# Kernel optimization log

Hardware: AMD Instinct MI355X
Metric: run time of the kernel (lower is better)

Reference implementation:

```python
import jax, jax.numpy as jnp
import numpy as np

N_NODES = 8192
GNN_DIM = 512
N_FEAT = 64
N_ITER = 4


def setup_inputs() -> dict:
    key = jax.random.key(0)
    ks = jax.random.split(key, 8)
    scale = 1.0 / np.sqrt(GNN_DIM)
    return {
        "labels": jax.random.normal(ks[0], (N_NODES, GNN_DIM), dtype=jnp.float32),
        "adj": jax.random.uniform(ks[1], (N_NODES, N_NODES), dtype=jnp.float32),
        "features": jax.random.normal(ks[2], (N_FEAT,), dtype=jnp.float32),
        "W_self": jax.random.normal(ks[3], (GNN_DIM, GNN_DIM), dtype=jnp.float32) * scale,
        "b_self": jax.random.normal(ks[4], (GNN_DIM,), dtype=jnp.float32) * scale,
        "W_neigh": jax.random.normal(ks[5], (GNN_DIM, GNN_DIM), dtype=jnp.float32) * scale,
        "W_fc": jax.random.normal(ks[6], (1, GNN_DIM + N_FEAT), dtype=jnp.float32) * scale,
        "b_fc": jax.random.normal(ks[7], (1,), dtype=jnp.float32) * scale,
    }


def reference(labels, adj, features, W_self, b_self, W_neigh, W_fc, b_fc):
    x = labels  # [N, D]
    for _ in range(N_ITER):
        acc = adj @ x                                   # [N, D] neighbor aggregation
        x = jax.nn.relu(x @ W_self.T + b_self + acc @ W_neigh.T)
    pooled = jnp.mean(x, axis=0)                        # [D]
    z = jnp.concatenate([pooled, features]) @ W_fc.T + b_fc  # [1]
    return jax.nn.sigmoid(z)
```

## Files before the change

kernel.cpp:

```cpp
#include <hip/hip_runtime.h>

typedef __bf16 bf16;
typedef bf16 bf16x8 __attribute__((ext_vector_type(8)));
typedef bf16 bf16x4 __attribute__((ext_vector_type(4)));
typedef float f32x4 __attribute__((ext_vector_type(4)));

constexpr int NN = 8192;
constexpr int DD = 512;
constexpr size_t PSZB = (size_t)NN * DD * 2;
constexpr size_t PSZE = (size_t)NN * DD;
constexpr int NS = 4;

static __device__ inline bf16x8 cvt8(const float* __restrict__ p) {
  f32x4 a = *(const f32x4*)p;
  f32x4 b = *(const f32x4*)(p + 4);
  bf16x8 r;
  r[0] = (bf16)a[0]; r[1] = (bf16)a[1]; r[2] = (bf16)a[2]; r[3] = (bf16)a[3];
  r[4] = (bf16)b[0]; r[5] = (bf16)b[1]; r[6] = (bf16)b[2]; r[7] = (bf16)b[3];
  return r;
}

#define GLDS(g, l) __builtin_amdgcn_global_load_lds( \
    (const __attribute__((address_space(1))) unsigned int*)(const void*)(g), \
    (__attribute__((address_space(3))) unsigned int*)(void*)(l), 16, 0, 0)


__global__ __launch_bounds__(256) void convert_w_kernel(
    const float* __restrict__ a, const float* __restrict__ b,
    bf16* __restrict__ ao, bf16* __restrict__ bo) {
  int i8 = ((int)blockIdx.x * 256 + (int)threadIdx.x) * 8;
  if (i8 < DD * DD) {
    *(bf16x8*)&ao[i8] = cvt8(a + i8);
  } else {
    int j = i8 - DD * DD;
    *(bf16x8*)&bo[j] = cvt8(b + j);
  }
}

__global__ __launch_bounds__(256) void convert_adj_kernel(
    const float* __restrict__ a, bf16* __restrict__ o) {
  size_t i8 = ((size_t)blockIdx.x * 256 + threadIdx.x) * 8;
  *(bf16x8*)&o[i8] = cvt8(a + i8);
}

__global__ __launch_bounds__(256) void convert_x_kernel(
    const float* __restrict__ src, bf16* __restrict__ xb, bf16* __restrict__ xbT) {
  __shared__ __align__(16) float tile[64][68];
  const int tid = (int)threadIdx.x;
  const int r0 = (int)blockIdx.x * 64;
  const int c0 = (int)blockIdx.y * 64;
#pragma unroll
  for (int p = 0; p < 4; ++p) {
    int row = p * 16 + (tid >> 4);
    int col = (tid & 15) * 4;
    *(f32x4*)&tile[row][col] = *(const f32x4*)&src[(size_t)(r0 + row) * DD + c0 + col];
  }
  __syncthreads();
#pragma unroll
  for (int p = 0; p < 4; ++p) {
    int row = p * 16 + (tid >> 4);
    int col = (tid & 15) * 4;
    f32x4 v = *(const f32x4*)&tile[row][col];
    bf16x4 o;
    o[0] = (bf16)v[0]; o[1] = (bf16)v[1]; o[2] = (bf16)v[2]; o[3] = (bf16)v[3];
    *(bf16x4*)&xb[(size_t)(r0 + row) * DD + c0 + col] = o;
  }
  {
    int c = tid >> 2;
    int rp = (tid & 3) * 16;
    bf16x8 o0, o1;
#pragma unroll
    for (int j = 0; j < 8; ++j) o0[j] = (bf16)tile[rp + j][c];
#pragma unroll
    for (int j = 0; j < 8; ++j) o1[j] = (bf16)tile[rp + 8 + j][c];
    *(bf16x8*)&xbT[(size_t)(c0 + c) * NN + r0 + rp] = o0;
    *(bf16x8*)&xbT[(size_t)(c0 + c) * NN + r0 + rp + 8] = o1;
  }
}


__device__ __forceinline__ void stage_half(const bf16* __restrict__ g, int grow0, int k0,
                                           bf16* smbase, int wave, int lane) {
#pragma unroll
  for (int i = 0; i < 2; ++i) {
    int c = wave * 2 + i;
    int row = grow0 + c * 8 + (lane >> 3);
    int col = k0 + (((lane & 7) ^ ((lane >> 3) & 7)) << 3);
    GLDS(g + (size_t)row * NN + col, smbase + c * 512);
  }
}

__global__ __launch_bounds__(512, 2)
void gemm1_kernel(const bf16* __restrict__ adjb, const bf16* __restrict__ xbT,
                  bf16* __restrict__ pbase) {
  __shared__ __align__(16) bf16 sm[65536];
  const int bid  = (int)blockIdx.x;
  const int xcd  = bid & 7, ii = bid >> 3;
  const int cb   = ii & 1;
  const int jj_  = xcd + 8 * (ii >> 1);
  const int p    = jj_ >> 2;
  const int s    = jj_ & 3;
  const int prow0 = p * 256;
  const int bcol0 = cb * 256;
  const int kb    = s * 2048;
  bf16* __restrict__ P = pbase + (size_t)s * PSZE;

  const int tid  = (int)threadIdx.x;
  const int lane = tid & 63;
  const int wave = tid >> 6;
  const int wr   = wave >> 2;
  const int wc   = wave & 3;
  const int fr   = lane & 15, fq = lane >> 4;

  f32x4 acc[8][4] = {};

#define A_OFF(par) ((par) * 32768)
#define B_OFF(par) ((par) * 32768 + 16384)
#define STAGE_A(tile, half, par) \
  stage_half(adjb, prow0 + (half) * 128, kb + ((tile) & 31) * 64, \
             sm + A_OFF(par) + (half) * 8192, wave, lane)
#define STAGE_B(tile, half, par) \
  stage_half(xbT, bcol0 + (half) * 128, kb + ((tile) & 31) * 64, \
             sm + B_OFF(par) + (half) * 8192, wave, lane)
#define BARRIER() __builtin_amdgcn_s_barrier(); __builtin_amdgcn_sched_barrier(0)

  STAGE_B(0, 0, 0); STAGE_B(0, 1, 0); STAGE_A(0, 0, 0); STAGE_A(0, 1, 0);
  STAGE_B(1, 0, 1); STAGE_B(1, 1, 1); STAGE_A(1, 0, 1);

  bf16x8 bv[2][4], af[2][2];

#define LOAD_B(par)                                                        \
  _Pragma("unroll") for (int kk = 0; kk < 2; ++kk)                         \
  _Pragma("unroll") for (int n = 0; n < 4; ++n) {                          \
    int rowl = wc * 64 + n * 16 + fr;                                      \
    int slot = (kk * 4 + fq) ^ (rowl & 7);                                 \
    bv[kk][n] = *(const bf16x8*)&sm[B_OFF(par) + rowl * 64 + slot * 8];    \
  }
#define LOAD_A(q, par)                                                     \
  _Pragma("unroll") for (int kk = 0; kk < 2; ++kk)                         \
  _Pragma("unroll") for (int j = 0; j < 2; ++j) {                          \
    int rowl = (q) * 64 + wr * 32 + j * 16 + fr;                           \
    int slot = (kk * 4 + fq) ^ (rowl & 7);                                 \
    af[kk][j] = *(const bf16x8*)&sm[A_OFF(par) + rowl * 64 + slot * 8];    \
  }
#define QMFMA(q)                                                           \
  __builtin_amdgcn_s_setprio(1);                                           \
  _Pragma("unroll") for (int kk = 0; kk < 2; ++kk)                         \
  _Pragma("unroll") for (int j = 0; j < 2; ++j)                            \
  _Pragma("unroll") for (int n = 0; n < 4; ++n)                            \
    acc[2 * (q) + j][n] = __builtin_amdgcn_mfma_f32_16x16x32_bf16(         \
        af[kk][j], bv[kk][n], acc[2 * (q) + j][n], 0, 0, 0);               \
  __builtin_amdgcn_s_setprio(0);

  int par = 0;
  for (int t = 0; t < 32; ++t, par ^= 1) {
    asm volatile("s_waitcnt vmcnt(6)" ::: "memory");
    BARRIER();
    LOAD_B(par);
    LOAD_A(0, par);
    STAGE_A(t + 1, 1, par ^ 1);
    QMFMA(0);
    LOAD_A(1, par);
    QMFMA(1);

    BARRIER();
    LOAD_A(2, par);
    STAGE_B(t + 2, 0, par);
    STAGE_B(t + 2, 1, par);
    STAGE_A(t + 2, 0, par);
    QMFMA(2);
    LOAD_A(3, par);
    QMFMA(3);
  }

#pragma unroll
  for (int m = 0; m < 8; ++m)
#pragma unroll
    for (int n = 0; n < 4; ++n)
#pragma unroll
      for (int r = 0; r < 4; ++r) {
        int row = prow0 + (m >> 1) * 64 + wr * 32 + (m & 1) * 16 + fq * 4 + r;
        int col = bcol0 + wc * 64 + n * 16 + fr;
        P[(size_t)row * DD + col] = (bf16)acc[m][n][r];
      }
#undef A_OFF
#undef B_OFF
#undef STAGE_A
#undef STAGE_B
#undef LOAD_B
#undef LOAD_A
#undef QMFMA
#undef BARRIER
}

__global__ __launch_bounds__(1024, 4)
void gemm2_kernel(const bf16* __restrict__ wsb, const bf16* __restrict__ wnb,
                  bf16* __restrict__ xb, const bf16* __restrict__ pbase,
                  const float* __restrict__ bself, bf16* __restrict__ xbT) {
  __shared__ __align__(16) char smem[139264];
  const int tid  = (int)threadIdx.x;
  const int lane = tid & 63;
  const int wave = tid >> 6;
  const int n0 = (int)blockIdx.x * 32;
  const int fr = lane & 15, fq = lane >> 4;
  const int srow = lane >> 3;
  const int scol = ((lane & 7) ^ (srow & 7)) * 8;
  const int fnode = tid >> 3, fks = tid & 7;

  f32x4 acc[2][2] = {};

  {
    bf16* la = (bf16*)smem;
#pragma unroll
    for (int c = 0; c < 4; ++c) {
      int chunk = wave * 4 + c;
      GLDS(wsb + (size_t)(chunk * 8 + srow) * DD + scol, &la[chunk * 512]);
    }
    if (wave < 4)
      GLDS(xb + (size_t)(n0 + wave * 8 + srow) * DD + scol,
           &((bf16*)(smem + 131072))[wave * 512]);
  }
  asm volatile("s_waitcnt vmcnt(0)" ::: "memory");
  __builtin_amdgcn_s_barrier();

  for (int t = 0; t < 16; ++t) {
    const int par = t & 1;
    bf16* la = (bf16*)(smem + par * 65536);
    bf16* lb = (bf16*)(smem + 131072 + par * 4096);

    bf16x8 fv0, fv1, fv2, fv3;
    bool fold = false;
    if (t < 15) {
      const int tn = t + 1, prn = tn >> 3, k0n = (tn & 7) * 64;
      const bf16* __restrict__ An = prn ? wnb : wsb;
      bf16* lan = (bf16*)(smem + (par ^ 1) * 65536);
#pragma unroll
      for (int c = 0; c < 4; ++c) {
        int chunk = wave * 4 + c;
        GLDS(An + (size_t)(chunk * 8 + srow) * DD + k0n + scol, &lan[chunk * 512]);
      }
      if (prn == 0) {
        if (wave < 4)
          GLDS(xb + (size_t)(n0 + wave * 8 + srow) * DD + k0n + scol,
               &((bf16*)(smem + 131072 + (par ^ 1) * 4096))[wave * 512]);
      } else if (tid < 256) {
        fold = true;
        const bf16* p0 = pbase + (size_t)(n0 + fnode) * DD + k0n + fks * 8;
        fv0 = *(const bf16x8*)(p0);
        fv1 = *(const bf16x8*)(p0 + PSZE);
        fv2 = *(const bf16x8*)(p0 + 2 * PSZE);
        fv3 = *(const bf16x8*)(p0 + 3 * PSZE);
      }
    }

    bf16x8 af[2][2], bv[2][2];
#pragma unroll
    for (int kk = 0; kk < 2; ++kk) {
#pragma unroll
      for (int m = 0; m < 2; ++m) {
        int rowl = wave * 32 + m * 16 + fr;
        int slot = (kk * 4 + fq) ^ (rowl & 7);
        af[kk][m] = *(const bf16x8*)&la[rowl * 64 + slot * 8];
      }
#pragma unroll
      for (int n = 0; n < 2; ++n) {
        int rowl = n * 16 + fr;
        int slot = (kk * 4 + fq) ^ (rowl & 7);
        bv[kk][n] = *(const bf16x8*)&lb[rowl * 64 + slot * 8];
      }
    }
#pragma unroll
    for (int kk = 0; kk < 2; ++kk)
#pragma unroll
      for (int m = 0; m < 2; ++m)
#pragma unroll
        for (int n = 0; n < 2; ++n)
          acc[m][n] = __builtin_amdgcn_mfma_f32_16x16x32_bf16(af[kk][m], bv[kk][n], acc[m][n], 0, 0, 0);

    if (fold) {
      bf16x8 o;
#pragma unroll
      for (int j = 0; j < 8; ++j)
        o[j] = (bf16)((float)fv0[j] + (float)fv1[j] + (float)fv2[j] + (float)fv3[j]);
      *(bf16x8*)&((bf16*)(smem + 131072 + (par ^ 1) * 4096))[fnode * 64 + (fks ^ (fnode & 7)) * 8] = o;
    }

    asm volatile("s_waitcnt vmcnt(0) lgkmcnt(0)" ::: "memory");
    __builtin_amdgcn_s_barrier();
  }

  bf16* lds_t = (bf16*)smem;
#pragma unroll
  for (int m = 0; m < 2; ++m)
#pragma unroll
    for (int n = 0; n < 2; ++n)
#pragma unroll
      for (int r = 0; r < 4; ++r) {
        int d = wave * 32 + m * 16 + fq * 4 + r;
        int node = n * 16 + fr;
        float v = acc[m][n][r] + bself[d];
        v = v > 0.f ? v : 0.f;
        bf16 h = (bf16)v;
        xbT[(size_t)d * NN + n0 + node] = h;
        lds_t[node * 520 + d] = h;
      }
  __syncthreads();
  {
    int node = tid >> 5;
    int dc = (tid & 31) * 16;
    bf16x8 v0 = *(const bf16x8*)&lds_t[node * 520 + dc];
    bf16x8 v1 = *(const bf16x8*)&lds_t[node * 520 + dc + 8];
    *(bf16x8*)&xb[(size_t)(n0 + node) * DD + dc] = v0;
    *(bf16x8*)&xb[(size_t)(n0 + node) * DD + dc + 8] = v1;
  }
}


__global__ __launch_bounds__(256) void pool_kernel(
    const bf16* __restrict__ xb, float* __restrict__ pooled) {
  const int t = (int)threadIdx.x;
  const int r0 = (int)blockIdx.x * 32;
  float s0 = 0.f, s1 = 0.f;
  for (int r = 0; r < 32; ++r) {
    s0 += (float)xb[(size_t)(r0 + r) * DD + t];
    s1 += (float)xb[(size_t)(r0 + r) * DD + t + 256];
  }
  atomicAdd(&pooled[t], s0);
  atomicAdd(&pooled[t + 256], s1);
}

__global__ __launch_bounds__(64) void final_kernel(
    const float* __restrict__ pooled, const float* __restrict__ features,
    const float* __restrict__ wfc, const float* __restrict__ bfc,
    float* __restrict__ out) {
  const int t = (int)threadIdx.x;
  float s = 0.f;
  for (int i = t; i < DD + 64; i += 64) {
    float v = (i < DD) ? pooled[i] * (1.0f / (float)NN) : features[i - DD];
    s += v * wfc[i];
  }
#pragma unroll
  for (int off = 32; off > 0; off >>= 1) s += __shfl_down(s, off);
  if (t == 0) {
    float z = s + bfc[0];
    out[0] = 1.0f / (1.0f + expf(-z));
  }
}


extern "C" void kernel_launch(void* const* d_in, const int* in_sizes, int n_in,
                              void* d_out, int out_size, void* d_ws, size_t ws_size,
                              hipStream_t stream) {
  const float* labels   = (const float*)d_in[0];
  const float* adj      = (const float*)d_in[1];
  const float* features = (const float*)d_in[2];
  const float* W_self   = (const float*)d_in[3];
  const float* b_self   = (const float*)d_in[4];
  const float* W_neigh  = (const float*)d_in[5];
  const float* W_fc     = (const float*)d_in[6];
  const float* b_fc     = (const float*)d_in[7];
  float* out = (float*)d_out;

  char* ws = (char*)d_ws;
  bf16*  xb    = (bf16*)(ws);
  bf16*  xbT   = (bf16*)(ws + PSZB);
  bf16*  pbase = (bf16*)(ws + 2 * PSZB);
  char*  after_p = ws + (size_t)(2 + NS) * PSZB;
  bf16*  wsb    = (bf16*)(after_p);
  bf16*  wnb    = (bf16*)(after_p + 524288);
  float* pooled = (float*)(after_p + 1048576);
  bf16*  adjb   = (bf16*)(after_p + 1048576 + 4096);

  convert_w_kernel<<<2 * DD * DD / 8 / 256, 256, 0, stream>>>(W_self, W_neigh, wsb, wnb);
  convert_adj_kernel<<<(int)((size_t)NN * NN / 8 / 256), 256, 0, stream>>>(adj, adjb);
  convert_x_kernel<<<dim3(NN / 64, DD / 64), 256, 0, stream>>>(labels, xb, xbT);

  for (int it = 0; it < 4; ++it) {
    gemm1_kernel<<<256, 512, 0, stream>>>(adjb, xbT, pbase);
    gemm2_kernel<<<NN / 32, 1024, 0, stream>>>(wsb, wnb, xb, pbase, b_self, xbT);
  }

  hipMemsetAsync(pooled, 0, DD * sizeof(float), stream);
  pool_kernel<<<NN / 32, 256, 0, stream>>>(xb, pooled);
  final_kernel<<<1, 64, 0, stream>>>(pooled, features, W_fc, b_fc, out);
}
```

Measured before the change: 421.6 us.

## Interleave global-to-LDS staging with MFMA quarters using per-phase barriers

Rewrites the main aggregation GEMM loop as a 2x-unrolled, eight-phase schedule. Each phase issues LDS fragment loads and one slice of global-to-LDS staging, then runs a barrier-fenced, high-priority MFMA cluster. Parity is now hard-coded per unrolled half, and the vmcnt waits are retuned so staging spreads evenly over the MFMA work. The goal is better overlap of memory traffic with matrix math and less issue contention. The cost is many more workgroup barriers per tile.

```diff
diff --git a/kernel.cpp b/kernel.cpp
--- a/kernel.cpp
+++ b/kernel.cpp
@@ -122,10 +122,9 @@
 #define STAGE_B(tile, half, par) \
   stage_half(xbT, bcol0 + (half) * 128, kb + ((tile) & 31) * 64, \
              sm + B_OFF(par) + (half) * 8192, wave, lane)
-#define BARRIER() __builtin_amdgcn_s_barrier(); __builtin_amdgcn_sched_barrier(0)
-
-  STAGE_B(0, 0, 0); STAGE_B(0, 1, 0); STAGE_A(0, 0, 0); STAGE_A(0, 1, 0);
-  STAGE_B(1, 0, 1); STAGE_B(1, 1, 1); STAGE_A(1, 0, 1);
+
+  STAGE_B(0, 0, 0); STAGE_B(0, 1, 0); STAGE_A(0, 0, 0);
+  STAGE_A(0, 1, 0); STAGE_B(1, 0, 1); STAGE_B(1, 1, 1); STAGE_A(1, 0, 1);
 
   bf16x8 bv[2][4], af[2][2];
 
@@ -144,33 +143,52 @@
     af[kk][j] = *(const bf16x8*)&sm[A_OFF(par) + rowl * 64 + slot * 8];    \
   }
 #define QMFMA(q)                                                           \
-  __builtin_amdgcn_s_setprio(1);                                           \
   _Pragma("unroll") for (int kk = 0; kk < 2; ++kk)                         \
   _Pragma("unroll") for (int j = 0; j < 2; ++j)                            \
   _Pragma("unroll") for (int n = 0; n < 4; ++n)                            \
     acc[2 * (q) + j][n] = __builtin_amdgcn_mfma_f32_16x16x32_bf16(         \
-        af[kk][j], bv[kk][n], acc[2 * (q) + j][n], 0, 0, 0);               \
-  __builtin_amdgcn_s_setprio(0);
-
-  int par = 0;
-  for (int t = 0; t < 32; ++t, par ^= 1) {
-    asm volatile("s_waitcnt vmcnt(6)" ::: "memory");
-    BARRIER();
-    LOAD_B(par);
-    LOAD_A(0, par);
-    STAGE_A(t + 1, 1, par ^ 1);
-    QMFMA(0);
-    LOAD_A(1, par);
-    QMFMA(1);
-
-    BARRIER();
-    LOAD_A(2, par);
-    STAGE_B(t + 2, 0, par);
-    STAGE_B(t + 2, 1, par);
-    STAGE_A(t + 2, 0, par);
-    QMFMA(2);
-    LOAD_A(3, par);
-    QMFMA(3);
+        af[kk][j], bv[kk][n], acc[2 * (q) + j][n], 0, 0, 0);
+#define PHASE_TAIL(q)                                                      \
+  __builtin_amdgcn_s_barrier();                                            \
+  asm volatile("s_waitcnt lgkmcnt(0)" ::: "memory");                       \
+  __builtin_amdgcn_sched_barrier(0);                                       \
+  __builtin_amdgcn_s_setprio(1);                                           \
+  QMFMA(q);                                                                \
+  __builtin_amdgcn_s_setprio(0);                                           \
+  __builtin_amdgcn_s_barrier();
+
+  for (int it = 0; it < 16; ++it) {
+    const int t = it * 2;
+    asm volatile("s_waitcnt vmcnt(8)" ::: "memory");
+    LOAD_B(0);
+    LOAD_A(0, 0);
+    STAGE_A(t + 1, 1, 1);
+    PHASE_TAIL(0);
+    LOAD_A(1, 0);
+    STAGE_B(t + 2, 0, 0);
+    PHASE_TAIL(1);
+    asm volatile("s_waitcnt vmcnt(10)" ::: "memory");
+    LOAD_A(2, 0);
+    STAGE_B(t + 2, 1, 0);
+    PHASE_TAIL(2);
+    LOAD_A(3, 0);
+    STAGE_A(t + 2, 0, 0);
+    PHASE_TAIL(3);
+    asm volatile("s_waitcnt vmcnt(8)" ::: "memory");
+    LOAD_B(1);
+    LOAD_A(0, 1);
+    STAGE_A(t + 2, 1, 0);
+    PHASE_TAIL(0);
+    LOAD_A(1, 1);
+    STAGE_B(t + 3, 0, 1);
+    PHASE_TAIL(1);
+    asm volatile("s_waitcnt vmcnt(10)" ::: "memory");
+    LOAD_A(2, 1);
+    STAGE_B(t + 3, 1, 1);
+    PHASE_TAIL(2);
+    LOAD_A(3, 1);
+    STAGE_A(t + 3, 0, 1);
+    PHASE_TAIL(3);
   }
 
 #pragma unroll
@@ -190,7 +208,7 @@
 #undef LOAD_B
 #undef LOAD_A
 #undef QMFMA
-#undef BARRIER
+#undef PHASE_TAIL
 }
 
 __global__ __launch_bounds__(1024, 4)
```

Result: faster. 411.8 us (-2.3%).
